# Optimization experiments

Measured on AMD Instinct MI355X. Metric: run time of the kernel, lower is better.

The kernel has to match this reference:

```python
import jax, jax.numpy as jnp
import numpy as np

D_MODEL = 768; HEADS = 8; LAYERS = 2

def pos_encoding(n, d):
    pos = np.arange(n, dtype=np.float32)[:, None]
    div = np.exp(np.arange(0, d, 2, dtype=np.float32) * -(np.log(10000.0) / d))
    pe = np.zeros((n, d), np.float32)
    pe[:, 0::2] = np.sin(pos * div)
    pe[:, 1::2] = np.cos(pos * div)
    return jnp.asarray(pe)

def layer_norm(x, g, b):
    m = x.mean(-1, keepdims=True)
    v = ((x - m) ** 2).mean(-1, keepdims=True)
    return (x - m) / jnp.sqrt(v + 1e-6) * g + b

def mha(k_in, v_in, q_in, mask, Wq, bq, Wk, bk, Wv, bv, Wout, bout):
    # BertSum MultiHeadedAttention(key, value, query, mask); mask True = blocked
    B, Lq, d = q_in.shape
    dk = d // HEADS
    def proj(x, W, b):
        y = x @ W + b
        return y.reshape(B, x.shape[1], HEADS, dk).transpose(0, 2, 1, 3)
    q = proj(q_in, Wq, bq)
    k = proj(k_in, Wk, bk)
    v = proj(v_in, Wv, bv)
    scores = jnp.einsum('bhqd,bhkd->bhqk', q, k) / jnp.sqrt(jnp.float32(dk))
    scores = jnp.where(mask[:, None, :, :], jnp.float32(-1e18), scores)
    attn = jax.nn.softmax(scores, axis=-1)
    out = jnp.einsum('bhqk,bhkd->bhqd', attn, v).transpose(0, 2, 1, 3).reshape(B, Lq, d)
    return out @ Wout + bout

def ffn(x, W1, b1, W2, b2, g, b):
    # PositionwiseFeedForward: x + w2(gelu(w1(LN(x))))
    return x + jax.nn.gelu(layer_norm(x, g, b) @ W1 + b1) @ W2 + b2

def setup_inputs():
    key = jax.random.key(0)
    ks = jax.random.split(key, 20)
    B, N_TOP, N_OUT, D, DFF, DH = 8, 512, 64, D_MODEL, 3072, 512
    s = 0.02
    return {
        'top_vecs': jax.random.normal(ks[0], (B, N_TOP, D), jnp.float32),
        'inputs': jax.random.normal(ks[1], (B, N_OUT, D), jnp.float32),
        'mask': jnp.ones((B, N_TOP), bool),
        'label_mask': jnp.ones((B, N_OUT), bool),
        'Wq': jax.random.normal(ks[2], (LAYERS, D, D)) * s,
        'bq': jnp.zeros((LAYERS, D)),
        'Wk': jax.random.normal(ks[3], (LAYERS, D, D)) * s,
        'bk': jnp.zeros((LAYERS, D)),
        'Wv': jax.random.normal(ks[4], (LAYERS, D, D)) * s,
        'bv': jnp.zeros((LAYERS, D)),
        'Wout': jax.random.normal(ks[5], (LAYERS, D, D)) * s,
        'bout': jnp.zeros((LAYERS, D)),
        'W1': jax.random.normal(ks[6], (LAYERS, D, DFF)) * s,
        'b1': jnp.zeros((LAYERS, DFF)),
        'W2': jax.random.normal(ks[7], (LAYERS, DFF, D)) * s,
        'b2': jnp.zeros((LAYERS, D)),
        'ln_g': jnp.ones((LAYERS, D)),
        'ln_b': jnp.zeros((LAYERS, D)),
        'Wo': jax.random.normal(ks[8], (D, DH)) * s,
        'bo': jnp.zeros((DH,)),
        'Wi': jax.random.normal(ks[9], (D, DH)) * s,
        'bi': jnp.zeros((DH,)),
        'v_w': jax.random.normal(ks[10], (DH,)) * s,
        'v_b': jnp.zeros(()),
    }

def reference(top_vecs, inputs, mask, label_mask, Wq, bq, Wk, bk, Wv, bv, Wout, bout,
              W1, b1, W2, b2, ln_g, ln_b, Wo, bo, Wi, bi, v_w, v_b):
    B, n_out, d = inputs.shape
    pe = pos_encoding(n_out, d)
    seq_mask = jnp.triu(jnp.ones((n_out, n_out), bool), 1)  # future positions blocked
    self_mask = (~label_mask)[:, None, :] | seq_mask[None]  # (B, n_out, n_out)
    ctx_mask = jnp.broadcast_to((~mask)[:, None, :], (B, n_out, mask.shape[1]))
    x = inputs + pe[None]
    for i in range(LAYERS):
        ctx = mha(x, x, x, self_mask, Wq[i], bq[i], Wk[i], bk[i], Wv[i], bv[i], Wout[i], bout[i])
        dec = mha(top_vecs, top_vecs, ctx, ctx_mask, Wq[i], bq[i], Wk[i], bk[i], Wv[i], bv[i], Wout[i], bout[i])
        x = ffn(dec, W1[i], b1[i], W2[i], b2[i], ln_g[i], ln_b[i])
    # additive-attention scoring head: (B, n_out, n_top, d_hidden) broadcast intermediate
    h = jax.nn.leaky_relu((x @ Wo + bo)[:, :, None, :] + (top_vecs @ Wi + bi)[:, None, :, :])
    scores = jnp.einsum('bonh,h->bon', h, v_w) + v_b
    return jax.nn.softmax(scores, axis=-1)
```

## Files before the change

### kernel.cpp

```cpp
#include <hip/hip_runtime.h>
#include <math.h>

#define D_MODEL 768
#define HEADS   8
#define DK      96
#define NB      8
#define N_TOP   512
#define N_OUT   64
#define DFF     3072
#define DH      512

typedef short  short8  __attribute__((ext_vector_type(8)));
typedef short  short4v __attribute__((ext_vector_type(4)));
typedef float  floatx4 __attribute__((ext_vector_type(4)));

__device__ __forceinline__ unsigned short f2bf(float f) {
    unsigned int u = __float_as_uint(f);
    u += 0x7fffu + ((u >> 16) & 1u);
    return (unsigned short)(u >> 16);
}
__device__ __forceinline__ float bf2f(unsigned short h) {
    return __uint_as_float(((unsigned int)h) << 16);
}

__device__ __forceinline__ float gelu_f(float x) {
    const float c = 0.7978845608028654f;
    return 0.5f * x * (1.0f + tanhf(c * (x + 0.044715f * x * x * x)));
}

__device__ __forceinline__ void gl16(const short* g, short* l) {
    __builtin_amdgcn_global_load_lds(
        (const __attribute__((address_space(1))) void*)g,
        (__attribute__((address_space(3))) void*)l, 16, 0, 0);
}

__device__ __forceinline__ float block_reduce_sum(float v, float* red) {
    int tid = threadIdx.x;
    red[tid] = v;
    __syncthreads();
    for (int s = blockDim.x >> 1; s > 0; s >>= 1) {
        if (tid < s) red[tid] += red[tid + s];
        __syncthreads();
    }
    float r = red[0];
    __syncthreads();
    return r;
}
__device__ __forceinline__ float block_reduce_max(float v, float* red) {
    int tid = threadIdx.x;
    red[tid] = v;
    __syncthreads();
    for (int s = blockDim.x >> 1; s > 0; s >>= 1) {
        if (tid < s) red[tid] = fmaxf(red[tid], red[tid + s]);
        __syncthreads();
    }
    float r = red[0];
    __syncthreads();
    return r;
}

struct TPack {
    const float* src[14];
    short*       dst[14];
    int K[14], N[14];
    int tstart[15];
};

__global__ __launch_bounds__(256) void multi_transpose_kernel(TPack pk) {
    __shared__ float t[32][33];
    int tile = blockIdx.x;
    int i = 0;
    while (i < 13 && tile >= pk.tstart[i + 1]) ++i;
    int lt = tile - pk.tstart[i];
    int K = pk.K[i], N = pk.N[i];
    int ntx = N >> 5;
    int bx = lt % ntx, by = lt / ntx;
    const float* in = pk.src[i];
    short* out = pk.dst[i];
    int tx = threadIdx.x & 31, ty = threadIdx.x >> 5;
#pragma unroll
    for (int r = 0; r < 4; ++r)
        t[ty + r * 8][tx] = in[(size_t)(by * 32 + ty + r * 8) * N + bx * 32 + tx];
    __syncthreads();
#pragma unroll
    for (int r = 0; r < 4; ++r)
        out[(size_t)(bx * 32 + ty + r * 8) * K + by * 32 + tx] =
            (short)f2bf(t[tx][ty + r * 8]);
}

__global__ void prep_kernel(const float* __restrict__ top, const float* __restrict__ inp,
                            short* __restrict__ top_bf, short* __restrict__ xb,
                            int nkv4, int nx4) {
    int i = blockIdx.x * blockDim.x + threadIdx.x;
    if (i < nkv4) {
        float4 v = ((const float4*)top)[i];
        top_bf[i * 4 + 0] = (short)f2bf(v.x);
        top_bf[i * 4 + 1] = (short)f2bf(v.y);
        top_bf[i * 4 + 2] = (short)f2bf(v.z);
        top_bf[i * 4 + 3] = (short)f2bf(v.w);
        return;
    }
    int j = i - nkv4;
    if (j >= nx4) return;
#pragma unroll
    for (int u = 0; u < 4; ++u) {
        int idx = j * 4 + u;
        int c   = idx % D_MODEL;
        int pos = (idx / D_MODEL) % N_OUT;
        int jj  = c >> 1;
        float ang = (float)pos * expf((float)(2 * jj) * (-logf(10000.0f) / (float)D_MODEL));
        float pe  = (c & 1) ? cosf(ang) : sinf(ang);
        xb[idx] = (short)f2bf(inp[idx] + pe);
    }
}

struct GDesc {
    const short* A;
    const short* Bt;
    int K;
    int nbx;
    short*       dst[3];
    const float* bias[3];
    int cum[4];
    int vtlog[3];
    int nseg;
};
struct GPack {
    GDesc d[3];
    int start1, start2;
};

__global__ __launch_bounds__(256) void gemm128g_kernel(GPack gp) {
    __shared__ __align__(16) short As[2 * 128 * 32];
    __shared__ __align__(16) short Bs[2 * 128 * 32];

    const int blk = blockIdx.x;
    const int di = (blk >= gp.start1 ? 1 : 0) + (blk >= gp.start2 ? 1 : 0);
    const GDesc& D = gp.d[di];
    const int l = blk - (di == 0 ? 0 : (di == 1 ? gp.start1 : gp.start2));
    const int bm = (l / D.nbx) * 128, bn = (l % D.nbx) * 128;
    const int K = D.K;
    const int nst = K >> 5;

    const int tid  = threadIdx.x;
    const int wave = tid >> 6, lane = tid & 63;
    const int wr = wave >> 1, wc = wave & 1;
    const int lc = lane & 15;
    const int lq = lane >> 4;
    const int lr4 = lq * 4;
    const int ko  = lq * 8;

    const int srow = wave * 32 + (lane >> 2);
    const int scol = (lane & 3) * 8;
    const int sbase = wave * 1024;

    floatx4 acc[4][4];
#pragma unroll
    for (int i = 0; i < 4; ++i)
#pragma unroll
        for (int j = 0; j < 4; ++j) acc[i][j] = (floatx4)0.0f;

    const short* Ab = D.A  + (size_t)(bm + srow) * K + scol;
    const short* Bb = D.Bt + (size_t)(bn + srow) * K + scol;
    const size_t hq = (size_t)16 * K;

#define STG128(t, buf) do {                                   \
        const short* _a = Ab + (size_t)(t) * 32;              \
        const short* _b = Bb + (size_t)(t) * 32;              \
        short* _la = As + (buf) * 4096 + sbase;               \
        short* _lb = Bs + (buf) * 4096 + sbase;               \
        gl16(_a,      _la);                                   \
        gl16(_a + hq, _la + 512);                             \
        gl16(_b,      _lb);                                   \
        gl16(_b + hq, _lb + 512);                             \
    } while (0)

    STG128(0, 0);
    __syncthreads();

    int cur = 0;
    for (int t = 0; t < nst; ++t) {
        if (t + 1 < nst) STG128(t + 1, cur ^ 1);
        const short* Ar = As + cur * 4096;
        const short* Br = Bs + cur * 4096;
        short8 a[4], b[4];
#pragma unroll
        for (int f = 0; f < 4; ++f) {
            a[f] = *(const short8*)&Ar[(wr * 64 + f * 16 + lc) * 32 + ko];
            b[f] = *(const short8*)&Br[(wc * 64 + f * 16 + lc) * 32 + ko];
        }
#pragma unroll
        for (int fr = 0; fr < 4; ++fr)
#pragma unroll
            for (int fc = 0; fc < 4; ++fc)
                acc[fr][fc] = __builtin_amdgcn_mfma_f32_16x16x32_bf16(
                    a[fr], b[fc], acc[fr][fc], 0, 0, 0);
        __syncthreads();
        cur ^= 1;
    }
#undef STG128

#pragma unroll
    for (int fc = 0; fc < 4; ++fc) {
        int col = bn + wc * 64 + fc * 16 + lc;
        int s = 0;
        while (s + 1 < D.nseg && col >= D.cum[s + 1]) ++s;
        int cl   = col - D.cum[s];
        int segw = D.cum[s + 1] - D.cum[s];
        const float* bp = D.bias[s];
        short* dst = D.dst[s];
        int vtl = D.vtlog[s];
        float bi = bp ? bp[cl] : 0.0f;
#pragma unroll
        for (int fr = 0; fr < 4; ++fr)
#pragma unroll
            for (int r = 0; r < 4; ++r) {
                int row = bm + wr * 64 + fr * 16 + lr4 + r;
                float x = acc[fr][fc][r] + bi;
                if (vtl) {
                    int seq = 1 << vtl;
                    dst[((size_t)(row >> vtl) * segw + cl) * seq + (row & (seq - 1))] =
                        (short)f2bf(x);
                } else {
                    dst[(size_t)row * segw + cl] = (short)f2bf(x);
                }
            }
    }
}

__global__ __launch_bounds__(256) void gemm_bf16_kernel(
    const short* __restrict__ A, const short* __restrict__ Bt,
    const float* __restrict__ bias0, const float* __restrict__ bias1,
    const float* __restrict__ bias2, const float* __restrict__ residual,
    float* __restrict__ Cf, short* __restrict__ Cb0, short* __restrict__ Cb1,
    short* __restrict__ Cb2, float* __restrict__ part,
    int M, int N, int K, int act, int segw, int vt_seg, int vt_log) {
    __shared__ __align__(16) short As[2 * 2 * 64 * 32];
    __shared__ __align__(16) short Bs[2 * 2 * 64 * 32];

    const int bm = blockIdx.y * 64, bn = blockIdx.x * 64;
    const int nz = gridDim.z, kz = blockIdx.z;
    const int kchunk = K / nz;

    const int tid  = threadIdx.x;
    const int wave = tid >> 6, lane = tid & 63;
    const int wr = wave >> 1, wc = wave & 1;
    const int lc = lane & 15;
    const int lr4 = (lane >> 4) * 4;
    const int ko  = (lane >> 4) * 8;

    const int srow = wave * 16 + (lane >> 2);
    const int scol = (lane & 3) * 8;
    const int sbase = wave * 512;

    const int nst = kchunk >> 6;

    floatx4 acc[2][2];
#pragma unroll
    for (int i = 0; i < 2; ++i)
#pragma unroll
        for (int j = 0; j < 2; ++j) acc[i][j] = (floatx4)0.0f;

    const short* Ab = A  + (size_t)(bm + srow) * K + kz * kchunk + scol;
    const short* Bb = Bt + (size_t)(bn + srow) * K + kz * kchunk + scol;

#define STG64(t, buf) do {                                    \
        const short* _a = Ab + (size_t)(t) * 64;              \
        const short* _b = Bb + (size_t)(t) * 64;              \
        short* _la = As + (buf) * 4096 + sbase;               \
        short* _lb = Bs + (buf) * 4096 + sbase;               \
        gl16(_a,      _la);                                   \
        gl16(_a + 32, _la + 2048);                            \
        gl16(_b,      _lb);                                   \
        gl16(_b + 32, _lb + 2048);                            \
    } while (0)

    STG64(0, 0);
    __syncthreads();

    int cur = 0;
    for (int t = 0; t < nst; ++t) {
        if (t + 1 < nst) STG64(t + 1, cur ^ 1);
#pragma unroll
        for (int sub = 0; sub < 2; ++sub) {
            const short* Ar = As + cur * 4096 + sub * 2048;
            const short* Br = Bs + cur * 4096 + sub * 2048;
            short8 a0 = *(const short8*)&Ar[(wr * 32 + lc) * 32 + ko];
            short8 a1 = *(const short8*)&Ar[(wr * 32 + 16 + lc) * 32 + ko];
            short8 b0 = *(const short8*)&Br[(wc * 32 + lc) * 32 + ko];
            short8 b1 = *(const short8*)&Br[(wc * 32 + 16 + lc) * 32 + ko];
            acc[0][0] = __builtin_amdgcn_mfma_f32_16x16x32_bf16(a0, b0, acc[0][0], 0, 0, 0);
            acc[0][1] = __builtin_amdgcn_mfma_f32_16x16x32_bf16(a0, b1, acc[0][1], 0, 0, 0);
            acc[1][0] = __builtin_amdgcn_mfma_f32_16x16x32_bf16(a1, b0, acc[1][0], 0, 0, 0);
            acc[1][1] = __builtin_amdgcn_mfma_f32_16x16x32_bf16(a1, b1, acc[1][1], 0, 0, 0);
        }
        __syncthreads();
        cur ^= 1;
    }
#undef STG64

    if (nz > 1) {
        float* pt = part + (size_t)kz * M * N;
#pragma unroll
        for (int fr = 0; fr < 2; ++fr)
#pragma unroll
            for (int fc = 0; fc < 2; ++fc) {
                int col = bn + wc * 32 + fc * 16 + lc;
#pragma unroll
                for (int r = 0; r < 4; ++r) {
                    int row = bm + wr * 32 + fr * 16 + lr4 + r;
                    pt[(size_t)row * N + col] = acc[fr][fc][r];
                }
            }
        return;
    }

#pragma unroll
    for (int fr = 0; fr < 2; ++fr) {
#pragma unroll
        for (int fc = 0; fc < 2; ++fc) {
            int col = bn + wc * 32 + fc * 16 + lc;
            int seg = (col >= segw) + (col >= 2 * segw);
            int cl  = col - seg * segw;
            const float* bp = (seg == 0) ? bias0 : ((seg == 1) ? bias1 : bias2);
            short* dst      = (seg == 0) ? Cb0   : ((seg == 1) ? Cb1   : Cb2);
            float bi = bp ? bp[cl] : 0.0f;
#pragma unroll
            for (int r = 0; r < 4; ++r) {
                int row = bm + wr * 32 + fr * 16 + lr4 + r;
                float x = acc[fr][fc][r] + bi;
                if (residual) x += residual[(size_t)row * N + col];
                if (act == 1) x = gelu_f(x);
                if (Cf) Cf[(size_t)row * N + col] = x;
                if (dst) {
                    if (seg == vt_seg) {
                        int sq = 1 << vt_log;
                        dst[((size_t)(row >> vt_log) * segw + cl) * sq + (row & (sq - 1))] =
                            (short)f2bf(x);
                    } else {
                        dst[(size_t)row * segw + cl] = (short)f2bf(x);
                    }
                }
            }
        }
    }
}

__global__ __launch_bounds__(256) void combine_kernel(
    const float* __restrict__ part, int nz, int N, int MN,
    const float* __restrict__ bias, const float* __restrict__ residual,
    float* __restrict__ Cf, short* __restrict__ Cb) {
    int e = (blockIdx.x * 256 + threadIdx.x) * 4;
    float4 s = *(const float4*)(part + e);
    for (int z = 1; z < nz; ++z) {
        float4 p = *(const float4*)(part + (size_t)z * MN + e);
        s.x += p.x; s.y += p.y; s.z += p.z; s.w += p.w;
    }
    int col = e % N;
    float4 b4 = *(const float4*)(bias + col);
    s.x += b4.x; s.y += b4.y; s.z += b4.z; s.w += b4.w;
    if (residual) {
        float4 r4 = *(const float4*)(residual + e);
        s.x += r4.x; s.y += r4.y; s.z += r4.z; s.w += r4.w;
    }
    if (Cf) *(float4*)(Cf + e) = s;
    if (Cb) {
        short4v o;
        o[0] = (short)f2bf(s.x); o[1] = (short)f2bf(s.y);
        o[2] = (short)f2bf(s.z); o[3] = (short)f2bf(s.w);
        *(short4v*)(Cb + e) = o;
    }
}

__global__ __launch_bounds__(256) void combine_ln_kernel(
    const float* __restrict__ part, int nz,
    const float* __restrict__ bias, const float* __restrict__ g,
    const float* __restrict__ bln,
    float* __restrict__ dec, short* __restrict__ lno) {
    __shared__ float red[256];
    const int MN = 512 * D_MODEL;
    int row = blockIdx.x, tid = threadIdx.x;
    float x[3];
    float s = 0.0f;
#pragma unroll
    for (int i = 0; i < 3; ++i) {
        int c = tid + i * 256;
        float v = bias[c];
        for (int z = 0; z < nz; ++z)
            v += part[(size_t)z * MN + (size_t)row * D_MODEL + c];
        x[i] = v; s += v;
        dec[(size_t)row * D_MODEL + c] = v;
    }
    float mean = block_reduce_sum(s, red) * (1.0f / D_MODEL);
    float vs = 0.0f;
#pragma unroll
    for (int i = 0; i < 3; ++i) {
        float d = x[i] - mean;
        vs += d * d;
    }
    float var = block_reduce_sum(vs, red) * (1.0f / D_MODEL);
    float inv = 1.0f / sqrtf(var + 1e-6f);
#pragma unroll
    for (int i = 0; i < 3; ++i) {
        int c = tid + i * 256;
        lno[(size_t)row * D_MODEL + c] = (short)f2bf((x[i] - mean) * inv * g[c] + bln[c]);
    }
}

template<int LK, bool CAUSAL>
__global__ __launch_bounds__(64) void attn_mfma_kernel(
    const short* __restrict__ Q, const short* __restrict__ K,
    const short* __restrict__ VT, short* __restrict__ out) {
    constexpr int NF = LK / 16;
    constexpr int KS = LK / 32;
    __shared__ __align__(16) short P[16][LK + 8];

    int idx = blockIdx.x;
    const int w = idx & 3;  idx >>= 2;
    const int h = idx & 7;  idx >>= 3;
    const int b = idx;
    const int lane = threadIdx.x;
    const int lc = lane & 15;
    const int lq = lane >> 4;
    const int ko = lq * 8;

    short8 qf[3];
    const short* qbase = Q + ((size_t)(b * N_OUT + w * 16 + lc)) * D_MODEL + h * DK;
#pragma unroll
    for (int s = 0; s < 3; ++s) qf[s] = *(const short8*)(qbase + s * 32 + ko);

    floatx4 acc[NF];
#pragma unroll
    for (int f = 0; f < NF; ++f) acc[f] = (floatx4)0.0f;
    const short* kbase = K + ((size_t)(b * LK)) * D_MODEL + h * DK;
#pragma unroll
    for (int f = 0; f < NF; ++f) {
        const short* kr = kbase + (size_t)(f * 16 + lc) * D_MODEL;
#pragma unroll
        for (int s = 0; s < 3; ++s) {
            short8 kf = *(const short8*)(kr + s * 32 + ko);
            acc[f] = __builtin_amdgcn_mfma_f32_16x16x32_bf16(qf[s], kf, acc[f], 0, 0, 0);
        }
    }

    const float scale = 0.10206207261596575f;
    float inv[4];
#pragma unroll
    for (int r = 0; r < 4; ++r) {
        int row = w * 16 + lq * 4 + r;
        float m = -INFINITY;
#pragma unroll
        for (int f = 0; f < NF; ++f) {
            float s = acc[f][r] * scale;
            if (CAUSAL && (f * 16 + lc) > row) s = -INFINITY;
            acc[f][r] = s;
            m = fmaxf(m, s);
        }
#pragma unroll
        for (int d = 1; d < 16; d <<= 1) m = fmaxf(m, __shfl_xor(m, d));
        float sum = 0.0f;
#pragma unroll
        for (int f = 0; f < NF; ++f) {
            float e = expf(acc[f][r] - m);
            acc[f][r] = e;
            sum += e;
        }
#pragma unroll
        for (int d = 1; d < 16; d <<= 1) sum += __shfl_xor(sum, d);
        inv[r] = 1.0f / sum;
    }

#pragma unroll
    for (int f = 0; f < NF; ++f)
#pragma unroll
        for (int r = 0; r < 4; ++r)
            P[lq * 4 + r][f * 16 + lc] = (short)f2bf(acc[f][r] * inv[r]);
    __syncthreads();

    floatx4 oacc[6];
#pragma unroll
    for (int n = 0; n < 6; ++n) oacc[n] = (floatx4)0.0f;
    const short* vbase = VT + ((size_t)b * D_MODEL + h * DK) * LK;
#pragma unroll
    for (int s = 0; s < KS; ++s) {
        short8 pf = *(const short8*)&P[lc][s * 32 + ko];
#pragma unroll
        for (int n = 0; n < 6; ++n) {
            short8 vf = *(const short8*)(vbase + (size_t)(n * 16 + lc) * LK + s * 32 + ko);
            oacc[n] = __builtin_amdgcn_mfma_f32_16x16x32_bf16(pf, vf, oacc[n], 0, 0, 0);
        }
    }

#pragma unroll
    for (int n = 0; n < 6; ++n)
#pragma unroll
        for (int r = 0; r < 4; ++r) {
            int row = b * N_OUT + w * 16 + lq * 4 + r;
            int col = h * DK + n * 16 + lc;
            out[(size_t)row * D_MODEL + col] = (short)f2bf(oacc[n][r]);
        }
}

__global__ __launch_bounds__(256) void attn_cross_kernel(
    const short* __restrict__ Q, const short* __restrict__ K,
    const short* __restrict__ VT, short* __restrict__ out) {
    constexpr int LK = 512, KW = 128, NF = KW / 16, KS = KW / 32;
    __shared__ __align__(16) short P[4][16][KW + 8];
    __shared__ float Of[4][16][96];
    __shared__ float ms[4][16];
    __shared__ float ss[4][16];

    int idx = blockIdx.x;
    const int w = idx & 3;  idx >>= 2;
    const int h = idx & 7;  idx >>= 3;
    const int b = idx;
    const int tid  = threadIdx.x;
    const int ws   = tid >> 6;
    const int lane = tid & 63;
    const int lc = lane & 15;
    const int lq = lane >> 4;
    const int ko = lq * 8;

    short8 qf[3];
    const short* qbase = Q + ((size_t)(b * N_OUT + w * 16 + lc)) * D_MODEL + h * DK;
#pragma unroll
    for (int s = 0; s < 3; ++s) qf[s] = *(const short8*)(qbase + s * 32 + ko);

    floatx4 acc[NF];
#pragma unroll
    for (int f = 0; f < NF; ++f) acc[f] = (floatx4)0.0f;
    const short* kbase = K + ((size_t)(b * LK + ws * KW)) * D_MODEL + h * DK;
#pragma unroll
    for (int f = 0; f < NF; ++f) {
        const short* kr = kbase + (size_t)(f * 16 + lc) * D_MODEL;
#pragma unroll
        for (int s = 0; s < 3; ++s) {
            short8 kf = *(const short8*)(kr + s * 32 + ko);
            acc[f] = __builtin_amdgcn_mfma_f32_16x16x32_bf16(qf[s], kf, acc[f], 0, 0, 0);
        }
    }

    const float scale = 0.10206207261596575f;
#pragma unroll
    for (int r = 0; r < 4; ++r) {
        float m = -INFINITY;
#pragma unroll
        for (int f = 0; f < NF; ++f) {
            float s = acc[f][r] * scale;
            acc[f][r] = s;
            m = fmaxf(m, s);
        }
#pragma unroll
        for (int d = 1; d < 16; d <<= 1) m = fmaxf(m, __shfl_xor(m, d));
        float sum = 0.0f;
#pragma unroll
        for (int f = 0; f < NF; ++f) {
            float e = expf(acc[f][r] - m);
            acc[f][r] = e;
            sum += e;
        }
#pragma unroll
        for (int d = 1; d < 16; d <<= 1) sum += __shfl_xor(sum, d);
        if (lc == 0) {
            ms[ws][lq * 4 + r] = m;
            ss[ws][lq * 4 + r] = sum;
        }
    }

#pragma unroll
    for (int f = 0; f < NF; ++f)
#pragma unroll
        for (int r = 0; r < 4; ++r)
            P[ws][lq * 4 + r][f * 16 + lc] = (short)f2bf(acc[f][r]);
    __syncthreads();

    floatx4 oacc[6];
#pragma unroll
    for (int n = 0; n < 6; ++n) oacc[n] = (floatx4)0.0f;
    const short* vbase = VT + ((size_t)b * D_MODEL + h * DK) * LK + ws * KW;
#pragma unroll
    for (int s = 0; s < KS; ++s) {
        short8 pf = *(const short8*)&P[ws][lc][s * 32 + ko];
#pragma unroll
        for (int n = 0; n < 6; ++n) {
            short8 vf = *(const short8*)(vbase + (size_t)(n * 16 + lc) * LK + s * 32 + ko);
            oacc[n] = __builtin_amdgcn_mfma_f32_16x16x32_bf16(pf, vf, oacc[n], 0, 0, 0);
        }
    }

#pragma unroll
    for (int n = 0; n < 6; ++n)
#pragma unroll
        for (int r = 0; r < 4; ++r)
            Of[ws][lq * 4 + r][n * 16 + lc] = oacc[n][r];
    __syncthreads();

    for (int e = tid; e < 16 * 96; e += 256) {
        int row = e / 96, col = e - row * 96;
        float m0 = ms[0][row], m1 = ms[1][row], m2 = ms[2][row], m3 = ms[3][row];
        float m = fmaxf(fmaxf(m0, m1), fmaxf(m2, m3));
        float f0 = expf(m0 - m), f1 = expf(m1 - m);
        float f2 = expf(m2 - m), f3 = expf(m3 - m);
        float denom = f0 * ss[0][row] + f1 * ss[1][row] +
                      f2 * ss[2][row] + f3 * ss[3][row];
        float val = f0 * Of[0][row][col] + f1 * Of[1][row][col] +
                    f2 * Of[2][row][col] + f3 * Of[3][row][col];
        out[(size_t)(b * N_OUT + w * 16 + row) * D_MODEL + h * DK + col] =
            (short)f2bf(val / denom);
    }
}

__global__ __launch_bounds__(512) void head_kernel(
    const float* __restrict__ a, const short* __restrict__ cb,
    const float* __restrict__ v_w, const float* __restrict__ v_b,
    float* __restrict__ out) {
    __shared__ float as[DH];
    __shared__ float vs[DH];
    __shared__ float red[512];

    int b = blockIdx.x >> 6;
    int o = blockIdx.x & 63;
    int tid = threadIdx.x;

    as[tid] = a[((size_t)b * N_OUT + o) * DH + tid];
    vs[tid] = v_w[tid];
    __syncthreads();

    const short* crow = cb + ((size_t)b * N_TOP + tid) * DH;
    float s0 = 0.0f, s1 = 0.0f, s2 = 0.0f, s3 = 0.0f;
#pragma unroll 2
    for (int hh = 0; hh < DH; hh += 32) {
        short8 c0 = *(const short8*)(crow + hh);
        short8 c1 = *(const short8*)(crow + hh + 8);
        short8 c2 = *(const short8*)(crow + hh + 16);
        short8 c3 = *(const short8*)(crow + hh + 24);
#pragma unroll
        for (int u = 0; u < 8; ++u) {
            float x0 = as[hh + u]      + bf2f((unsigned short)c0[u]);
            float x1 = as[hh + 8 + u]  + bf2f((unsigned short)c1[u]);
            float x2 = as[hh + 16 + u] + bf2f((unsigned short)c2[u]);
            float x3 = as[hh + 24 + u] + bf2f((unsigned short)c3[u]);
            x0 = fmaxf(x0, 0.0f) + 0.01f * fminf(x0, 0.0f);
            x1 = fmaxf(x1, 0.0f) + 0.01f * fminf(x1, 0.0f);
            x2 = fmaxf(x2, 0.0f) + 0.01f * fminf(x2, 0.0f);
            x3 = fmaxf(x3, 0.0f) + 0.01f * fminf(x3, 0.0f);
            s0 = fmaf(vs[hh + u], x0, s0);
            s1 = fmaf(vs[hh + 8 + u], x1, s1);
            s2 = fmaf(vs[hh + 16 + u], x2, s2);
            s3 = fmaf(vs[hh + 24 + u], x3, s3);
        }
    }
    float s = (s0 + s1) + (s2 + s3) + v_b[0];

    float m = block_reduce_max(s, red);
    float e = expf(s - m);
    float sum = block_reduce_sum(e, red);
    out[((size_t)b * N_OUT + o) * N_TOP + tid] = e / sum;
}

extern "C" void kernel_launch(void* const* d_in, const int* in_sizes, int n_in,
                              void* d_out, int out_size, void* d_ws, size_t ws_size,
                              hipStream_t stream) {
    const float* top  = (const float*)d_in[0];
    const float* inp  = (const float*)d_in[1];
    const float* Wq   = (const float*)d_in[4];
    const float* bq   = (const float*)d_in[5];
    const float* Wk   = (const float*)d_in[6];
    const float* bk   = (const float*)d_in[7];
    const float* Wv   = (const float*)d_in[8];
    const float* bv   = (const float*)d_in[9];
    const float* Wout = (const float*)d_in[10];
    const float* bout = (const float*)d_in[11];
    const float* W1   = (const float*)d_in[12];
    const float* b1   = (const float*)d_in[13];
    const float* W2   = (const float*)d_in[14];
    const float* b2   = (const float*)d_in[15];
    const float* ln_g = (const float*)d_in[16];
    const float* ln_b = (const float*)d_in[17];
    const float* Wo   = (const float*)d_in[18];
    const float* bo   = (const float*)d_in[19];
    const float* Wi   = (const float*)d_in[20];
    const float* bi   = (const float*)d_in[21];
    const float* v_w  = (const float*)d_in[22];
    const float* v_b  = (const float*)d_in[23];

    char* p = (char*)d_ws;
    auto alloc = [&](size_t bytes) -> void* {
        void* r = (void*)p;
        p += (bytes + 255) & ~(size_t)255;
        return r;
    };

    const size_t WSQ = 768 * 768;
    short *WT_q[2], *WT_k[2], *WT_v[2], *WT_o[2], *WT_1[2], *WT_2[2];
    for (int L = 0; L < 2; ++L) {
        WT_q[L] = (short*)alloc(WSQ * 2);
        WT_k[L] = (short*)alloc(WSQ * 2);
        WT_v[L] = (short*)alloc(WSQ * 2);
        WT_o[L] = (short*)alloc(WSQ * 2);
        WT_1[L] = (short*)alloc((size_t)768 * DFF * 2);
        WT_2[L] = (short*)alloc((size_t)768 * DFF * 2);
    }
    short* WT_oh = (short*)alloc((size_t)768 * DH * 2);
    short* WT_ih = (short*)alloc((size_t)768 * DH * 2);

    const int NX  = NB * N_OUT * D_MODEL;
    const int NKV = NB * N_TOP * D_MODEL;

    short* top_bf = (short*)alloc((size_t)NKV * 2);
    short* X_bf   = (short*)alloc((size_t)NX * 2);
    short* Q_bf   = (short*)alloc((size_t)NX * 2);
    short* K_bf   = (short*)alloc((size_t)NKV * 2);
    short* VT     = (short*)alloc((size_t)NKV * 2);
    short* AO_bf  = (short*)alloc((size_t)NX * 2);
    short* CTX_bf = (short*)alloc((size_t)NX * 2);
    float* DEC    = (float*)alloc((size_t)NX * 4);
    short* LNO_bf = (short*)alloc((size_t)NX * 2);
    short* MID_bf = (short*)alloc((size_t)NB * N_OUT * DFF * 2);
    float* a_h    = (float*)alloc((size_t)NB * N_OUT * DH * 4);
    short* c_hb   = (short*)alloc((size_t)NB * N_TOP * DH * 2);
    float* PART   = (float*)alloc((size_t)4 * NX * 4);

    TPack pk;
    {
        int i = 0, t = 0;
        auto put = [&](const float* s, short* d, int K, int N) {
            pk.src[i] = s; pk.dst[i] = d; pk.K[i] = K; pk.N[i] = N;
            pk.tstart[i] = t; t += (K / 32) * (N / 32); ++i;
        };
        for (int L = 0; L < 2; ++L) {
            put(Wq + (size_t)L * WSQ, WT_q[L], 768, 768);
            put(Wk + (size_t)L * WSQ, WT_k[L], 768, 768);
            put(Wv + (size_t)L * WSQ, WT_v[L], 768, 768);
            put(Wout + (size_t)L * WSQ, WT_o[L], 768, 768);
            put(W1 + (size_t)L * 768 * DFF, WT_1[L], 768, DFF);
            put(W2 + (size_t)L * DFF * 768, WT_2[L], DFF, 768);
        }
        put(Wo, WT_oh, 768, DH);
        put(Wi, WT_ih, 768, DH);
        pk.tstart[14] = t;
        hipLaunchKernelGGL(multi_transpose_kernel, dim3(t), dim3(256), 0, stream, pk);
    }

    hipLaunchKernelGGL(prep_kernel, dim3((NKV / 4 + NX / 4 + 255) / 256), dim3(256),
                       0, stream, top, inp, top_bf, X_bf, NKV / 4, NX / 4);

    const int MQ = NB * N_OUT;
    const int MT = NB * N_TOP;

    auto G = [&](const short* A, const short* Bt,
                 const float* b0, const float* res, float* Cf, short* C0,
                 int M, int N, int K, int act) {
        hipLaunchKernelGGL(gemm_bf16_kernel, dim3(N / 64, M / 64, 1), dim3(256), 0, stream,
                           A, Bt, b0, nullptr, nullptr, res, Cf, C0, nullptr, nullptr,
                           nullptr, M, N, K, act, N, -1, 0);
    };
    auto GS = [&](const short* A, const short* Bt, const float* b0,
                  const float* res, float* Cf, short* C0,
                  int M, int N, int K, int nz) {
        hipLaunchKernelGGL(gemm_bf16_kernel, dim3(N / 64, M / 64, nz), dim3(256), 0, stream,
                           A, Bt, nullptr, nullptr, nullptr, nullptr,
                           nullptr, nullptr, nullptr, nullptr, PART,
                           M, N, K, 0, N, -1, 0);
        hipLaunchKernelGGL(combine_kernel, dim3(M * N / 1024), dim3(256), 0, stream,
                           PART, nz, N, M * N, b0, res, Cf, C0);
    };

    for (int L = 0; L < 2; ++L) {
        const float* _bq = bq + (size_t)L * D_MODEL;
        const float* _bk = bk + (size_t)L * D_MODEL;
        const float* _bv = bv + (size_t)L * D_MODEL;
        const float* _bo = bout + (size_t)L * D_MODEL;
        const float* _b1 = b1 + (size_t)L * DFF;
        const float* _b2 = b2 + (size_t)L * D_MODEL;
        const float* _g  = ln_g + (size_t)L * D_MODEL;
        const float* _b  = ln_b + (size_t)L * D_MODEL;

        {
            GPack gp{};
            gp.d[0].A = top_bf; gp.d[0].Bt = WT_k[L]; gp.d[0].K = D_MODEL;
            gp.d[0].nbx = 1536 / 128;
            gp.d[0].dst[0] = K_bf; gp.d[0].bias[0] = _bk; gp.d[0].vtlog[0] = 0;
            gp.d[0].dst[1] = VT;   gp.d[0].bias[1] = _bv; gp.d[0].vtlog[1] = 9;
            gp.d[0].cum[0] = 0; gp.d[0].cum[1] = 768; gp.d[0].cum[2] = 1536;
            gp.d[0].nseg = 2;
            int nb0 = (MT / 128) * gp.d[0].nbx;
            gp.d[1].A = X_bf; gp.d[1].Bt = WT_q[L]; gp.d[1].K = D_MODEL;
            gp.d[1].nbx = 2304 / 128;
            gp.d[1].dst[0] = Q_bf;   gp.d[1].bias[0] = _bq; gp.d[1].vtlog[0] = 0;
            gp.d[1].dst[1] = LNO_bf; gp.d[1].bias[1] = _bk; gp.d[1].vtlog[1] = 0;
            gp.d[1].dst[2] = MID_bf; gp.d[1].bias[2] = _bv; gp.d[1].vtlog[2] = 6;
            gp.d[1].cum[0] = 0; gp.d[1].cum[1] = 768; gp.d[1].cum[2] = 1536;
            gp.d[1].cum[3] = 2304; gp.d[1].nseg = 3;
            int nb1 = (MQ / 128) * gp.d[1].nbx;
            gp.start1 = nb0;
            int total = nb0 + nb1;
            if (L == 0) {
                gp.d[2].A = top_bf; gp.d[2].Bt = WT_ih; gp.d[2].K = D_MODEL;
                gp.d[2].nbx = DH / 128;
                gp.d[2].dst[0] = c_hb; gp.d[2].bias[0] = bi; gp.d[2].vtlog[0] = 0;
                gp.d[2].cum[0] = 0; gp.d[2].cum[1] = DH; gp.d[2].nseg = 1;
                gp.start2 = total;
                total += (MT / 128) * gp.d[2].nbx;
            } else {
                gp.start2 = 1 << 30;
            }
            hipLaunchKernelGGL(gemm128g_kernel, dim3(total), dim3(256), 0, stream, gp);
        }

        hipLaunchKernelGGL((attn_mfma_kernel<64, true>), dim3(NB * HEADS * 4), dim3(64),
                           0, stream, Q_bf, LNO_bf, MID_bf, AO_bf);
        GS(AO_bf, WT_o[L], _bo, nullptr, nullptr, CTX_bf, MQ, D_MODEL, D_MODEL, 3);

        GS(CTX_bf, WT_q[L], _bq, nullptr, nullptr, Q_bf, MQ, D_MODEL, D_MODEL, 3);
        hipLaunchKernelGGL(attn_cross_kernel, dim3(NB * HEADS * 4), dim3(256),
                           0, stream, Q_bf, K_bf, VT, AO_bf);
        hipLaunchKernelGGL(gemm_bf16_kernel, dim3(D_MODEL / 64, MQ / 64, 3), dim3(256),
                           0, stream, AO_bf, WT_o[L],
                           nullptr, nullptr, nullptr, nullptr,
                           nullptr, nullptr, nullptr, nullptr, PART,
                           MQ, D_MODEL, D_MODEL, 0, D_MODEL, -1, 0);
        hipLaunchKernelGGL(combine_ln_kernel, dim3(MQ), dim3(256), 0, stream,
                           PART, 3, _bo, _g, _b, DEC, LNO_bf);

        G(LNO_bf, WT_1[L], _b1, nullptr, nullptr, MID_bf, MQ, DFF, D_MODEL, 1);
        GS(MID_bf, WT_2[L], _b2, DEC, nullptr, X_bf, MQ, D_MODEL, DFF, 4);
    }

    GS(X_bf, WT_oh, bo, nullptr, a_h, nullptr, MQ, DH, D_MODEL, 3);
    hipLaunchKernelGGL(head_kernel, dim3(NB * N_OUT), dim3(512), 0, stream,
                       a_h, c_hb, v_w, v_b, (float*)d_out);
}
```

Measured before the change: 437.6 us.

## Fold Wout·Wq into one matrix, deepen gemm K-stage, fuse head split-K reduce

The self-attention output projection and the next query projection are folded algebraically. A precomputed WQC = WT_q·WT_o product and a combined bias replace two chained GEMMs with one per layer. The 128-tile grouped GEMM now stages 64 K-elements per pipeline step instead of 32, doubling LDS use to halve barrier count. The final head projection writes split-K partials that head_kernel sums with bias directly, and the transpose packing of W2/Wo/Wi is restructured. The weight fold adds per-call preprocessing kernels (a GEMM and a bias matvec) and an extra bf16 rounding of the fused matrix.

```diff
diff --git a/kernel.cpp b/kernel.cpp
--- a/kernel.cpp
+++ b/kernel.cpp
@@ -112,6 +112,24 @@
         float pe  = (c & 1) ? cosf(ang) : sinf(ang);
         xb[idx] = (short)f2bf(inp[idx] + pe);
     }
+}
+
+__global__ __launch_bounds__(256) void bqc_kernel(
+    const short* __restrict__ WTq0, const short* __restrict__ WTq1,
+    const float* __restrict__ bout, const float* __restrict__ bq,
+    float* __restrict__ bqc) {
+    int g = blockIdx.x * 256 + threadIdx.x;
+    int L = g / D_MODEL, n = g % D_MODEL;
+    const short* wr = (L == 0 ? WTq0 : WTq1) + (size_t)n * D_MODEL;
+    const float* bo_ = bout + (size_t)L * D_MODEL;
+    float s = bq[(size_t)L * D_MODEL + n];
+    for (int k = 0; k < D_MODEL; k += 8) {
+        short8 w = *(const short8*)(wr + k);
+#pragma unroll
+        for (int u = 0; u < 8; ++u)
+            s += bo_[k + u] * bf2f((unsigned short)w[u]);
+    }
+    bqc[(size_t)L * D_MODEL + n] = s;
 }
 
 struct GDesc {
@@ -131,8 +149,8 @@
 };
 
 __global__ __launch_bounds__(256) void gemm128g_kernel(GPack gp) {
-    __shared__ __align__(16) short As[2 * 128 * 32];
-    __shared__ __align__(16) short Bs[2 * 128 * 32];
+    __shared__ __align__(16) short As[2 * 2 * 128 * 32];
+    __shared__ __align__(16) short Bs[2 * 2 * 128 * 32];
 
     const int blk = blockIdx.x;
     const int di = (blk >= gp.start1 ? 1 : 0) + (blk >= gp.start2 ? 1 : 0);
@@ -140,7 +158,7 @@
     const int l = blk - (di == 0 ? 0 : (di == 1 ? gp.start1 : gp.start2));
     const int bm = (l / D.nbx) * 128, bn = (l % D.nbx) * 128;
     const int K = D.K;
-    const int nst = K >> 5;
+    const int nst = K >> 6;
 
     const int tid  = threadIdx.x;
     const int wave = tid >> 6, lane = tid & 63;
@@ -165,14 +183,18 @@
     const size_t hq = (size_t)16 * K;
 
 #define STG128(t, buf) do {                                   \
-        const short* _a = Ab + (size_t)(t) * 32;              \
-        const short* _b = Bb + (size_t)(t) * 32;              \
-        short* _la = As + (buf) * 4096 + sbase;               \
-        short* _lb = Bs + (buf) * 4096 + sbase;               \
-        gl16(_a,      _la);                                   \
-        gl16(_a + hq, _la + 512);                             \
-        gl16(_b,      _lb);                                   \
-        gl16(_b + hq, _lb + 512);                             \
+        const short* _a = Ab + (size_t)(t) * 64;              \
+        const short* _b = Bb + (size_t)(t) * 64;              \
+        short* _la = As + (buf) * 8192 + sbase;               \
+        short* _lb = Bs + (buf) * 8192 + sbase;               \
+        gl16(_a,           _la);                              \
+        gl16(_a + hq,      _la + 512);                        \
+        gl16(_a + 32,      _la + 4096);                       \
+        gl16(_a + 32 + hq, _la + 4096 + 512);                 \
+        gl16(_b,           _lb);                              \
+        gl16(_b + hq,      _lb + 512);                        \
+        gl16(_b + 32,      _lb + 4096);                       \
+        gl16(_b + 32 + hq, _lb + 4096 + 512);                 \
     } while (0)
 
     STG128(0, 0);
@@ -181,20 +203,23 @@
     int cur = 0;
     for (int t = 0; t < nst; ++t) {
         if (t + 1 < nst) STG128(t + 1, cur ^ 1);
-        const short* Ar = As + cur * 4096;
-        const short* Br = Bs + cur * 4096;
-        short8 a[4], b[4];
-#pragma unroll
-        for (int f = 0; f < 4; ++f) {
-            a[f] = *(const short8*)&Ar[(wr * 64 + f * 16 + lc) * 32 + ko];
-            b[f] = *(const short8*)&Br[(wc * 64 + f * 16 + lc) * 32 + ko];
-        }
-#pragma unroll
-        for (int fr = 0; fr < 4; ++fr)
-#pragma unroll
-            for (int fc = 0; fc < 4; ++fc)
-                acc[fr][fc] = __builtin_amdgcn_mfma_f32_16x16x32_bf16(
-                    a[fr], b[fc], acc[fr][fc], 0, 0, 0);
+#pragma unroll
+        for (int sub = 0; sub < 2; ++sub) {
+            const short* Ar = As + cur * 8192 + sub * 4096;
+            const short* Br = Bs + cur * 8192 + sub * 4096;
+            short8 a[4], b[4];
+#pragma unroll
+            for (int f = 0; f < 4; ++f) {
+                a[f] = *(const short8*)&Ar[(wr * 64 + f * 16 + lc) * 32 + ko];
+                b[f] = *(const short8*)&Br[(wc * 64 + f * 16 + lc) * 32 + ko];
+            }
+#pragma unroll
+            for (int fr = 0; fr < 4; ++fr)
+#pragma unroll
+                for (int fc = 0; fc < 4; ++fc)
+                    acc[fr][fc] = __builtin_amdgcn_mfma_f32_16x16x32_bf16(
+                        a[fr], b[fc], acc[fr][fc], 0, 0, 0);
+        }
         __syncthreads();
         cur ^= 1;
     }
@@ -611,7 +636,8 @@
 }
 
 __global__ __launch_bounds__(512) void head_kernel(
-    const float* __restrict__ a, const short* __restrict__ cb,
+    const float* __restrict__ part, const float* __restrict__ bo,
+    const short* __restrict__ cb,
     const float* __restrict__ v_w, const float* __restrict__ v_b,
     float* __restrict__ out) {
     __shared__ float as[DH];
@@ -622,7 +648,9 @@
     int o = blockIdx.x & 63;
     int tid = threadIdx.x;
 
-    as[tid] = a[((size_t)b * N_OUT + o) * DH + tid];
+    const int MN = 512 * DH;
+    int idx = blockIdx.x * DH + tid;
+    as[tid] = part[idx] + part[MN + idx] + part[2 * MN + idx] + bo[tid];
     vs[tid] = v_w[tid];
     __syncthreads();
 
@@ -703,6 +731,10 @@
     }
     short* WT_oh = (short*)alloc((size_t)768 * DH * 2);
     short* WT_ih = (short*)alloc((size_t)768 * DH * 2);
+    short* WQC[2];
+    WQC[0] = (short*)alloc(WSQ * 2);
+    WQC[1] = (short*)alloc(WSQ * 2);
+    float* BQC = (float*)alloc(2 * D_MODEL * 4);
 
     const int NX  = NB * N_OUT * D_MODEL;
     const int NKV = NB * N_TOP * D_MODEL;
@@ -713,11 +745,9 @@
     short* K_bf   = (short*)alloc((size_t)NKV * 2);
     short* VT     = (short*)alloc((size_t)NKV * 2);
     short* AO_bf  = (short*)alloc((size_t)NX * 2);
-    short* CTX_bf = (short*)alloc((size_t)NX * 2);
     float* DEC    = (float*)alloc((size_t)NX * 4);
     short* LNO_bf = (short*)alloc((size_t)NX * 2);
     short* MID_bf = (short*)alloc((size_t)NB * N_OUT * DFF * 2);
-    float* a_h    = (float*)alloc((size_t)NB * N_OUT * DH * 4);
     short* c_hb   = (short*)alloc((size_t)NB * N_TOP * DH * 2);
     float* PART   = (float*)alloc((size_t)4 * NX * 4);
 
@@ -734,16 +764,38 @@
             put(Wv + (size_t)L * WSQ, WT_v[L], 768, 768);
             put(Wout + (size_t)L * WSQ, WT_o[L], 768, 768);
             put(W1 + (size_t)L * 768 * DFF, WT_1[L], 768, DFF);
-            put(W2 + (size_t)L * DFF * 768, WT_2[L], DFF, 768);
-        }
-        put(Wo, WT_oh, 768, DH);
-        put(Wi, WT_ih, 768, DH);
+            put(W2 + (size_t)L * DFF * 768, WT_2[L], 768 * 4, 768);
+        }
+        pk.K[5] = DFF; pk.N[5] = 768;
+        pk.K[11] = DFF; pk.N[11] = 768;
+        t = 0;
+        for (int j = 0; j < 12; ++j) { pk.tstart[j] = t; t += (pk.K[j] / 32) * (pk.N[j] / 32); }
+        pk.src[12] = Wo; pk.dst[12] = WT_oh; pk.K[12] = 768; pk.N[12] = DH;
+        pk.tstart[12] = t; t += (768 / 32) * (DH / 32);
+        pk.src[13] = Wi; pk.dst[13] = WT_ih; pk.K[13] = 768; pk.N[13] = DH;
+        pk.tstart[13] = t; t += (768 / 32) * (DH / 32);
         pk.tstart[14] = t;
         hipLaunchKernelGGL(multi_transpose_kernel, dim3(t), dim3(256), 0, stream, pk);
     }
 
     hipLaunchKernelGGL(prep_kernel, dim3((NKV / 4 + NX / 4 + 255) / 256), dim3(256),
                        0, stream, top, inp, top_bf, X_bf, NKV / 4, NX / 4);
+
+    {
+        GPack gp{};
+        for (int L = 0; L < 2; ++L) {
+            gp.d[L].A = WT_q[L]; gp.d[L].Bt = WT_o[L]; gp.d[L].K = D_MODEL;
+            gp.d[L].nbx = 768 / 128;
+            gp.d[L].dst[0] = WQC[L]; gp.d[L].bias[0] = nullptr; gp.d[L].vtlog[0] = 0;
+            gp.d[L].cum[0] = 0; gp.d[L].cum[1] = 768;
+            gp.d[L].nseg = 1;
+        }
+        gp.start1 = 36;
+        gp.start2 = 1 << 30;
+        hipLaunchKernelGGL(gemm128g_kernel, dim3(72), dim3(256), 0, stream, gp);
+    }
+    hipLaunchKernelGGL(bqc_kernel, dim3(2 * D_MODEL / 256), dim3(256), 0, stream,
+                       WT_q[0], WT_q[1], bout, bq, BQC);
 
     const int MQ = NB * N_OUT;
     const int MT = NB * N_TOP;
@@ -810,9 +862,10 @@
 
         hipLaunchKernelGGL((attn_mfma_kernel<64, true>), dim3(NB * HEADS * 4), dim3(64),
                            0, stream, Q_bf, LNO_bf, MID_bf, AO_bf);
-        GS(AO_bf, WT_o[L], _bo, nullptr, nullptr, CTX_bf, MQ, D_MODEL, D_MODEL, 3);
-
-        GS(CTX_bf, WT_q[L], _bq, nullptr, nullptr, Q_bf, MQ, D_MODEL, D_MODEL, 3);
+
+        GS(AO_bf, WQC[L], BQC + (size_t)L * D_MODEL, nullptr, nullptr, Q_bf,
+           MQ, D_MODEL, D_MODEL, 3);
+
         hipLaunchKernelGGL(attn_cross_kernel, dim3(NB * HEADS * 4), dim3(256),
                            0, stream, Q_bf, K_bf, VT, AO_bf);
         hipLaunchKernelGGL(gemm_bf16_kernel, dim3(D_MODEL / 64, MQ / 64, 3), dim3(256),
@@ -827,7 +880,10 @@
         GS(MID_bf, WT_2[L], _b2, DEC, nullptr, X_bf, MQ, D_MODEL, DFF, 4);
     }
 
-    GS(X_bf, WT_oh, bo, nullptr, a_h, nullptr, MQ, DH, D_MODEL, 3);
+    hipLaunchKernelGGL(gemm_bf16_kernel, dim3(DH / 64, MQ / 64, 3), dim3(256), 0, stream,
+                       X_bf, WT_oh, nullptr, nullptr, nullptr, nullptr,
+                       nullptr, nullptr, nullptr, nullptr, PART,
+                       MQ, DH, D_MODEL, 0, DH, -1, 0);
     hipLaunchKernelGGL(head_kernel, dim3(NB * N_OUT), dim3(512), 0, stream,
-                       a_h, c_hb, v_w, v_b, (float*)d_out);
-}
+                       PART, bo, c_hb, v_w, v_b, (float*)d_out);
+}
```

Result: slower. 452.5 us (+3.4%).
